# Optimization experiments

Hardware: AMD Instinct MI355X
Metric: run time of the kernel (lower is better)

Reference implementation:

```python
import jax, jax.numpy as jnp
import numpy as np

FEATURE_DIM = 512
NUM_NODES = 50
NUM_GCN_LAYERS = 2
H_IMG = W_IMG = 256


def setup_inputs() -> dict:
    key = jax.random.key(0)
    ks = jax.random.split(key, 14)
    s = lambda k, shape: (jax.random.normal(k, shape, jnp.float32) * 0.02)
    return {
        "fts": jax.random.normal(ks[0], (1, FEATURE_DIM, H_IMG, W_IMG), jnp.float32),
        "msk": jax.random.randint(ks[1], (1, H_IMG, W_IMG), 0, 2, jnp.int32),
        "gcn_w": s(ks[2], (NUM_GCN_LAYERS, FEATURE_DIM, FEATURE_DIM)),
        "gcn_b": s(ks[3], (NUM_GCN_LAYERS, FEATURE_DIM)),
        "q_w": s(ks[4], (FEATURE_DIM // 2, FEATURE_DIM)),
        "q_b": s(ks[5], (FEATURE_DIM // 2,)),
        "k_w": s(ks[6], (FEATURE_DIM // 2, FEATURE_DIM)),
        "k_b": s(ks[7], (FEATURE_DIM // 2,)),
        "v_w": s(ks[8], (FEATURE_DIM, FEATURE_DIM)),
        "v_b": s(ks[9], (FEATURE_DIM,)),
        "map_w": s(ks[10], (FEATURE_DIM, FEATURE_DIM)),
        "map_b": s(ks[11], (FEATURE_DIM,)),
        "gamma": jnp.float32(0.1),   # torch inits to 0; nonzero for coverage
        "alpha": jnp.float32(-4.0),  # matches torch init
    }


def _adaptive_avg_pool1d(x, n):
    """torch.nn.AdaptiveAvgPool1d over last axis. x: [C, L] -> [C, n].
    Bin i averages x[:, floor(i*L/n) : ceil((i+1)*L/n)]. Done via cumsum."""
    L = x.shape[-1]
    i = np.arange(n)
    starts = (i * L) // n
    ends = ((i + 1) * L + n - 1) // n  # ceil
    cs = jnp.concatenate([jnp.zeros(x.shape[:-1] + (1,), x.dtype), jnp.cumsum(x, axis=-1)], axis=-1)
    sums = cs[..., ends] - cs[..., starts]
    return sums / jnp.asarray(ends - starts, x.dtype)


def reference(fts, msk, gcn_w, gcn_b, q_w, q_b, k_w, k_b, v_w, v_b, map_w, map_b, gamma, alpha):
    # interpolate(fts, size=msk.shape[-2:]) is identity: sizes already match.
    msk_f = msk.astype(fts.dtype)                     # [1, H, W]
    m = msk_f[:, None]                                # [1, 1, H, W]
    glob_proto = jnp.sum(fts * m, axis=(-2, -1)) / (jnp.sum(msk_f) + 1e-8)  # [1, 512]

    # masked_select -> [512, L] foreground pixels (eager nonzero; msk is data)
    fg_idx = jnp.nonzero(msk.reshape(-1))[0]
    fg = fts.reshape(FEATURE_DIM, -1)[:, fg_idx]      # [512, L]
    local_protos = _adaptive_avg_pool1d(fg, NUM_NODES).T  # [50, 512]

    H = jnp.concatenate([glob_proto, local_protos], axis=0)  # [51, 512]
    for l in range(NUM_GCN_LAYERS):
        Hn = H / jnp.maximum(jnp.linalg.norm(H, axis=1, keepdims=True), 1e-12)
        adj = jax.nn.softmax(jnp.maximum(Hn @ Hn.T, 0.0), axis=1)  # [51, 51]
        agg = adj @ H
        H = H + jax.nn.relu(agg @ gcn_w[l].T + gcn_b[l])

    # cross-attention: q from node 0, k/v from remaining 50 nodes
    q_node, k_nodes = H[:1], H[1:]
    q = q_node @ q_w.T + q_b                          # [1, 256]
    k = k_nodes @ k_w.T + k_b                         # [50, 256]
    v = k_nodes @ v_w.T + v_b                         # [50, 512]
    attn = jax.nn.softmax((q @ k.T) / (q_w.shape[0] ** 0.5), axis=-1)
    final_proto = q_node + gamma * ((attn @ v) @ map_w.T + map_b)  # [1, 512]

    w = jax.nn.sigmoid(alpha)
    return glob_proto * (1 - w) + final_proto * w
```

## Files before the change

### kernel.cpp

```cpp
#include <hip/hip_runtime.h>

#define HW 65536
#define CDIM 512
#define NN 50
#define NROWS 51

__device__ __forceinline__ float wave_sum(float v) {
#pragma unroll
  for (int off = 32; off; off >>= 1) v += __shfl_xor(v, off, 64);
  return v;
}
__device__ __forceinline__ int wave_sum_i(int v) {
#pragma unroll
  for (int off = 32; off; off >>= 1) v += __shfl_xor(v, off, 64);
  return v;
}
__device__ __forceinline__ float wave_max(float v) {
#pragma unroll
  for (int off = 32; off; off >>= 1) v = fmaxf(v, __shfl_xor(v, off, 64));
  return v;
}

__global__ __launch_bounds__(256) void k_transpose(
    const float* g0, const float* g1, const float* qw, const float* kw,
    const float* vw, const float* mw,
    float* g0T, float* g1T, float* qwT, float* kwT, float* vwT, float* mwT) {
  const float* in; float* out; int rows, cols;
  switch (blockIdx.z) {
    case 0: in = g0; out = g0T; rows = 512; cols = 512; break;
    case 1: in = g1; out = g1T; rows = 512; cols = 512; break;
    case 2: in = qw; out = qwT; rows = 256; cols = 512; break;
    case 3: in = kw; out = kwT; rows = 256; cols = 512; break;
    case 4: in = vw; out = vwT; rows = 512; cols = 512; break;
    default: in = mw; out = mwT; rows = 512; cols = 512; break;
  }
  int c0 = blockIdx.x * 32, r0 = blockIdx.y * 32;
  if (r0 >= rows || c0 >= cols) return;
  __shared__ float tile[32][33];
  int tx = threadIdx.x, ty = threadIdx.y;
#pragma unroll
  for (int j = 0; j < 4; ++j)
    tile[ty + j * 8][tx] = in[(size_t)(r0 + ty + j * 8) * cols + c0 + tx];
  __syncthreads();
#pragma unroll
  for (int j = 0; j < 4; ++j)
    out[(size_t)(c0 + ty + j * 8) * rows + r0 + tx] = tile[tx][ty + j * 8];
}

__global__ __launch_bounds__(256) void k_count(const int* msk, int* blkcnt, float* seg) {
  int t = threadIdx.x, b = blockIdx.x;
  int g = b * 256 + t;
  if (g < NN * CDIM) seg[g] = 0.f;
  int g2 = g + 16384;
  if (g2 < NN * CDIM) seg[g2] = 0.f;
  int4 m = ((const int4*)msk)[g];
  int c = (m.x != 0) + (m.y != 0) + (m.z != 0) + (m.w != 0);
  c = wave_sum_i(c);
  __shared__ int wl[4];
  if ((t & 63) == 0) wl[t >> 6] = c;
  __syncthreads();
  if (t == 0) blkcnt[b] = wl[0] + wl[1] + wl[2] + wl[3];
}

__global__ void k_scan(const int* blkcnt, int* blkoff, int* meta) {
  int t = threadIdx.x;
  int c = blkcnt[t];
  int x = c;
#pragma unroll
  for (int d = 1; d < 64; d <<= 1) {
    int y = __shfl_up(x, d, 64);
    if (t >= d) x += y;
  }
  blkoff[t] = x - c;
  int L = __shfl(x, 63, 64);
  if (t == 0) meta[0] = L;
  if (t < NN) {
    long long Ll = L;
    int s = (int)((long long)t * Ll / NN);
    int e = (int)(((long long)(t + 1) * Ll + NN - 1) / NN);
    int sn = (int)((long long)(t + 1) * Ll / NN);
    meta[2 + t] = s;
    meta[2 + NN + t] = e - s;
    meta[2 + 2 * NN + t] = (t < NN - 1) ? (e > sn) : 0;
  }
}

__global__ __launch_bounds__(256) void k_rank(const int* msk, const int* blkoff,
                                              const int* meta, unsigned char* bin8, int* P) {
  int t = threadIdx.x, blk = blockIdx.x;
  int L = meta[0];
  __shared__ int sst[NN];
  __shared__ int wtot[4];
  if (t < NN) sst[t] = meta[2 + t];
  int4 m = ((const int4*)msk)[blk * 256 + t];
  int fl[4] = {m.x != 0, m.y != 0, m.z != 0, m.w != 0};
  int cnt = fl[0] + fl[1] + fl[2] + fl[3];
  int lane = t & 63, wv = t >> 6;
  int x = cnt;
#pragma unroll
  for (int d = 1; d < 64; d <<= 1) {
    int y = __shfl_up(x, d, 64);
    if (lane >= d) x += y;
  }
  if (lane == 63) wtot[wv] = x;
  __syncthreads();
  int base = blkoff[blk] + (x - cnt);
  for (int w = 0; w < wv; ++w) base += wtot[w];
  int p0 = blk * 1024 + t * 4;
  int r = base;
#pragma unroll
  for (int j = 0; j < 4; ++j) {
    int p = p0 + j;
    unsigned char bv = 255;
    if (fl[j]) {
      bv = (unsigned char)((long long)NN * r / L);
#pragma unroll 1
      for (int i = 0; i < NN; ++i)
        if (sst[i] == r) P[i] = p;
      r++;
    }
    bin8[p] = bv;
  }
}

__global__ __launch_bounds__(256) void k_seg(const float* __restrict__ fts,
                                             const unsigned char* __restrict__ bin8,
                                             float* __restrict__ seg) {
  int pb = blockIdx.x * 1024;
  int cwb = blockIdx.y * 64;
  int t = threadIdx.x, lane = t & 63, wv = t >> 6;
  __shared__ int sbm[2];
  if (t == 0) { sbm[0] = 255; sbm[1] = -1; }
  __syncthreads();
  uchar4 b4 = ((const uchar4*)bin8)[(pb >> 2) + t];
  int bb[4] = {b4.x, b4.y, b4.z, b4.w};
  int mn = 255, mx = -1;
#pragma unroll
  for (int j = 0; j < 4; ++j)
    if (bb[j] != 255) { mn = min(mn, bb[j]); mx = max(mx, bb[j]); }
  if (mn < 255) atomicMin(&sbm[0], mn);
  if (mx >= 0) atomicMax(&sbm[1], mx);
  __syncthreads();
  int bmin = sbm[0], bmax = sbm[1];
  if (bmax < 0) return;
  int cw = cwb + wv * 16;
  const float* base = fts + (size_t)cw * HW + pb + lane;
  const unsigned char* bp = bin8 + pb + lane;
  if (bmax - bmin <= 3) {
    float racc[16][4];
#pragma unroll
    for (int a = 0; a < 16; ++a)
#pragma unroll
      for (int j = 0; j < 4; ++j) racc[a][j] = 0.f;
#pragma unroll 1
    for (int it = 0; it < 16; ++it) {
      int b = bp[it * 64];
      int brel = b - bmin;
      bool k0 = brel == 0, k1 = brel == 1, k2 = brel == 2, k3 = brel == 3;
#pragma unroll
      for (int cs = 0; cs < 16; ++cs) {
        float v = base[(size_t)cs * HW + it * 64];
        racc[cs][0] += k0 ? v : 0.f;
        racc[cs][1] += k1 ? v : 0.f;
        racc[cs][2] += k2 ? v : 0.f;
        racc[cs][3] += k3 ? v : 0.f;
      }
    }
#pragma unroll 1
    for (int cs = 0; cs < 16; ++cs) {
#pragma unroll 1
      for (int j = 0; j < 4; ++j) {
        float v = wave_sum(racc[cs][j]);
        if (lane == 0 && v != 0.f) {
          int b = bmin + j;
          if (b < NN) atomicAdd(&seg[b * CDIM + cw + cs], v);
        }
      }
    }
  } else {
    for (int it = 0; it < 16; ++it) {
      int b = bp[it * 64];
      if (b == 255) continue;
      for (int cs = 0; cs < 16; ++cs) {
        float v = base[(size_t)cs * HW + it * 64];
        atomicAdd(&seg[b * CDIM + cw + cs], v);
      }
    }
  }
}

__global__ __launch_bounds__(512) void k_buildH(const float* fts, const float* seg,
                                                const int* meta, const int* P,
                                                float* glob, float* H, float* norms) {
  int r = blockIdx.x;
  int c = threadIdx.x;
  int L = meta[0];
  float h;
  if (r == 0) {
    float s = 0.f;
#pragma unroll 1
    for (int i = 0; i < NN; ++i) s += seg[i * CDIM + c];
    h = s / ((float)L + 1e-8f);
    glob[c] = h;
  } else {
    int i = r - 1;
    const int* cntv = meta + 2 + NN;
    const int* ov = meta + 2 + 2 * NN;
    float s = seg[i * CDIM + c];
    if (ov[i]) s += fts[(size_t)c * HW + P[i + 1]];
    h = s / fmaxf((float)cntv[i], 1.f);
  }
  H[r * CDIM + c] = h;
  float x = wave_sum(h * h);
  __shared__ float wsum[8];
  if ((c & 63) == 0) wsum[c >> 6] = x;
  __syncthreads();
  if (c == 0) {
    float s = 0.f;
    for (int w = 0; w < 8; ++w) s += wsum[w];
    norms[r] = fmaxf(sqrtf(s), 1e-12f);
  }
}

__global__ __launch_bounds__(256) void k_gcnA(const float* H, const float* norms, float* agg) {
  int a = blockIdx.x;
  int t = threadIdx.x, lane = t & 63, wv = t >> 6;
  __shared__ float sHa[CDIM];
  __shared__ float sadj[64];
  sHa[t] = H[a * CDIM + t];
  sHa[t + 256] = H[a * CDIM + t + 256];
  __syncthreads();
  float na = norms[a];
  for (int b = wv; b < NROWS; b += 4) {
    float d = 0.f;
#pragma unroll 2
    for (int k = lane; k < CDIM; k += 64) d += sHa[k] * H[b * CDIM + k];
    d = wave_sum(d);
    if (lane == 0) sadj[b] = fmaxf(d / (na * norms[b]), 0.f);
  }
  __syncthreads();
  if (t < 64) {
    float s = (t < NROWS) ? sadj[t] : -1e30f;
    float m = wave_max(s);
    float e = (t < NROWS) ? expf(s - m) : 0.f;
    float sum = wave_sum(e);
    if (t < NROWS) sadj[t] = e / sum;
  }
  __syncthreads();
  for (int c = t; c < CDIM; c += 256) {
    float acc = 0.f;
#pragma unroll 1
    for (int b = 0; b < NROWS; ++b) acc += sadj[b] * H[b * CDIM + c];
    agg[a * CDIM + c] = acc;
  }
}

__global__ __launch_bounds__(512) void k_gcnB(float* H, const float* agg,
                                              const float* WT, const float* bias,
                                              float* norms) {
  int r = blockIdx.x, c = threadIdx.x;
  __shared__ float sagg[CDIM];
  sagg[c] = agg[r * CDIM + c];
  __syncthreads();
  float acc = bias[c];
#pragma unroll 4
  for (int k = 0; k < CDIM; ++k) acc += sagg[k] * WT[k * CDIM + c];
  float h = H[r * CDIM + c] + fmaxf(acc, 0.f);
  H[r * CDIM + c] = h;
  float x = wave_sum(h * h);
  __shared__ float wsum[8];
  if ((c & 63) == 0) wsum[c >> 6] = x;
  __syncthreads();
  if (c == 0) {
    float s = 0.f;
    for (int w = 0; w < 8; ++w) s += wsum[w];
    norms[r] = fmaxf(sqrtf(s), 1e-12f);
  }
}

__global__ __launch_bounds__(256) void k_qkv(const float* H, const float* qwT,
                                             const float* kwT, const float* vwT,
                                             const float* qb, const float* kb, const float* vb,
                                             float* q, float* kk, float* vv) {
  int blk = blockIdx.x;
  int t = threadIdx.x;
  __shared__ float sh[CDIM];
  sh[t] = H[blk * CDIM + t];
  sh[t + 256] = H[blk * CDIM + t + 256];
  __syncthreads();
  if (blk == 0) {
    float acc = qb[t];
#pragma unroll 4
    for (int k = 0; k < CDIM; ++k) acc += sh[k] * qwT[k * 256 + t];
    q[t] = acc;
  } else {
    int i = blk - 1;
    float acc = kb[t];
#pragma unroll 4
    for (int k = 0; k < CDIM; ++k) acc += sh[k] * kwT[k * 256 + t];
    kk[i * 256 + t] = acc;
    float a0 = vb[t], a1 = vb[t + 256];
#pragma unroll 4
    for (int k = 0; k < CDIM; ++k) {
      float hv = sh[k];
      a0 += hv * vwT[k * CDIM + t];
      a1 += hv * vwT[k * CDIM + t + 256];
    }
    vv[i * CDIM + t] = a0;
    vv[i * CDIM + t + 256] = a1;
  }
}

__global__ __launch_bounds__(512) void k_final(const float* H, const float* glob,
                                               const float* q, const float* kk, const float* vv,
                                               const float* mapwT, const float* mapb,
                                               const float* gamma, const float* alpha,
                                               float* out) {
  int t = threadIdx.x, lane = t & 63, wv = t >> 6;
  __shared__ float sattn[64];
  __shared__ float sav[CDIM];
  for (int i = wv; i < NN; i += 8) {
    float d = 0.f;
#pragma unroll
    for (int k = lane; k < 256; k += 64) d += q[k] * kk[i * 256 + k];
    d = wave_sum(d);
    if (lane == 0) sattn[i] = d * (1.f / 16.f);
  }
  __syncthreads();
  if (t < 64) {
    float s = (t < NN) ? sattn[t] : -1e30f;
    float m = wave_max(s);
    float e = (t < NN) ? expf(s - m) : 0.f;
    float sum = wave_sum(e);
    if (t < NN) sattn[t] = e / sum;
  }
  __syncthreads();
  float av = 0.f;
#pragma unroll 1
  for (int i = 0; i < NN; ++i) av += sattn[i] * vv[i * CDIM + t];
  sav[t] = av;
  __syncthreads();
  float o = mapb[t];
#pragma unroll 4
  for (int k = 0; k < CDIM; ++k) o += sav[k] * mapwT[k * CDIM + t];
  float w = 1.f / (1.f + expf(-alpha[0]));
  float fp = H[t] + gamma[0] * o;
  out[t] = glob[t] * (1.f - w) + fp * w;
}

extern "C" void kernel_launch(void* const* d_in, const int* in_sizes, int n_in,
                              void* d_out, int out_size, void* d_ws, size_t ws_size,
                              hipStream_t stream) {
  const float* fts = (const float*)d_in[0];
  const int* msk = (const int*)d_in[1];
  const float* gcn_w = (const float*)d_in[2];
  const float* gcn_b = (const float*)d_in[3];
  const float* q_w = (const float*)d_in[4];
  const float* q_b = (const float*)d_in[5];
  const float* k_w = (const float*)d_in[6];
  const float* k_b = (const float*)d_in[7];
  const float* v_w = (const float*)d_in[8];
  const float* v_b = (const float*)d_in[9];
  const float* map_w = (const float*)d_in[10];
  const float* map_b = (const float*)d_in[11];
  const float* gamma = (const float*)d_in[12];
  const float* alpha = (const float*)d_in[13];
  float* out = (float*)d_out;

  char* w = (char*)d_ws;
  auto alloc = [&](size_t bytes) {
    char* p = w;
    w += (bytes + 255) & ~(size_t)255;
    return p;
  };
  float* g0T = (float*)alloc(512 * 512 * 4);
  float* g1T = (float*)alloc(512 * 512 * 4);
  float* qwT = (float*)alloc(512 * 256 * 4);
  float* kwT = (float*)alloc(512 * 256 * 4);
  float* vwT = (float*)alloc(512 * 512 * 4);
  float* mwT = (float*)alloc(512 * 512 * 4);
  int* blkcnt = (int*)alloc(64 * 4);
  int* blkoff = (int*)alloc(64 * 4);
  int* meta = (int*)alloc(160 * 4);
  int* P = (int*)alloc(NN * 4);
  unsigned char* bin8 = (unsigned char*)alloc(HW);
  float* seg = (float*)alloc(NN * CDIM * 4);
  float* glob = (float*)alloc(CDIM * 4);
  float* H = (float*)alloc(NROWS * CDIM * 4);
  float* norms = (float*)alloc(NROWS * 4);
  float* agg = (float*)alloc(NROWS * CDIM * 4);
  float* qv = (float*)alloc(256 * 4);
  float* kv = (float*)alloc(NN * 256 * 4);
  float* vv = (float*)alloc(NN * CDIM * 4);

  k_transpose<<<dim3(16, 16, 6), dim3(32, 8), 0, stream>>>(
      gcn_w, gcn_w + 512 * 512, q_w, k_w, v_w, map_w, g0T, g1T, qwT, kwT, vwT, mwT);
  k_count<<<64, 256, 0, stream>>>(msk, blkcnt, seg);
  k_scan<<<1, 64, 0, stream>>>(blkcnt, blkoff, meta);
  k_rank<<<64, 256, 0, stream>>>(msk, blkoff, meta, bin8, P);
  k_seg<<<dim3(64, 8), 256, 0, stream>>>(fts, bin8, seg);
  k_buildH<<<NROWS, 512, 0, stream>>>(fts, seg, meta, P, glob, H, norms);
  for (int l = 0; l < 2; ++l) {
    k_gcnA<<<NROWS, 256, 0, stream>>>(H, norms, agg);
    k_gcnB<<<NROWS, 512, 0, stream>>>(H, agg, l ? g1T : g0T, gcn_b + l * 512, norms);
  }
  k_qkv<<<NROWS, 256, 0, stream>>>(H, qwT, kwT, vwT, q_b, k_b, v_b, qv, kv, vv);
  k_final<<<1, 512, 0, stream>>>(H, glob, qv, kv, vv, mwT, map_b, gamma, alpha, out);
}
```

Measured before the change: 558.6 us.

## Fuse prep kernels, merge GCN stages, widen grids for seg and small GEMVs

Folds the mask count, seg zeroing and all weight transposes into one prep kernel, and moves the block scan inside k_rank. Pivot lookup becomes an O(1) index instead of a 50-entry loop. k_seg now uses 256-pixel blocks with float4 loads and wave-level min/max instead of shared atomics, giving four times more blocks. The two GCN kernels per layer merge into one and are split across four column slices, with ping-pong H buffers and atomic norm accumulation. qkv and final are also split over more blocks so the small GEMVs spread across more CUs. This cuts launch count and raises parallelism, but each GCN slice block recomputes the full adjacency and aggregation.

```diff
diff --git a/kernel.cpp b/kernel.cpp
--- a/kernel.cpp
+++ b/kernel.cpp
@@ -20,78 +20,94 @@
   for (int off = 32; off; off >>= 1) v = fmaxf(v, __shfl_xor(v, off, 64));
   return v;
 }
-
-__global__ __launch_bounds__(256) void k_transpose(
-    const float* g0, const float* g1, const float* qw, const float* kw,
-    const float* vw, const float* mw,
-    float* g0T, float* g1T, float* qwT, float* kwT, float* vwT, float* mwT) {
-  const float* in; float* out; int rows, cols;
-  switch (blockIdx.z) {
-    case 0: in = g0; out = g0T; rows = 512; cols = 512; break;
-    case 1: in = g1; out = g1T; rows = 512; cols = 512; break;
-    case 2: in = qw; out = qwT; rows = 256; cols = 512; break;
-    case 3: in = kw; out = kwT; rows = 256; cols = 512; break;
-    case 4: in = vw; out = vwT; rows = 512; cols = 512; break;
-    default: in = mw; out = mwT; rows = 512; cols = 512; break;
-  }
-  int c0 = blockIdx.x * 32, r0 = blockIdx.y * 32;
-  if (r0 >= rows || c0 >= cols) return;
+__device__ __forceinline__ int wave_max_i(int v) {
+#pragma unroll
+  for (int off = 32; off; off >>= 1) v = max(v, __shfl_xor(v, off, 64));
+  return v;
+}
+__device__ __forceinline__ int wave_min_i(int v) {
+#pragma unroll
+  for (int off = 32; off; off >>= 1) v = min(v, __shfl_xor(v, off, 64));
+  return v;
+}
+
+__global__ __launch_bounds__(256) void k_prep(
+    const int* __restrict__ msk, int* __restrict__ blkcnt, float* __restrict__ seg,
+    float* __restrict__ nsqB, float* __restrict__ nsqC,
+    const float* __restrict__ g0, const float* __restrict__ g1,
+    const float* __restrict__ qw, const float* __restrict__ kw,
+    const float* __restrict__ vw, const float* __restrict__ mw,
+    float* __restrict__ g0T, float* __restrict__ g1T, float* __restrict__ qwT,
+    float* __restrict__ kwT, float* __restrict__ vwT, float* __restrict__ mwT) {
+  int t = threadIdx.x, b = blockIdx.x;
   __shared__ float tile[32][33];
-  int tx = threadIdx.x, ty = threadIdx.y;
-#pragma unroll
-  for (int j = 0; j < 4; ++j)
-    tile[ty + j * 8][tx] = in[(size_t)(r0 + ty + j * 8) * cols + c0 + tx];
-  __syncthreads();
-#pragma unroll
-  for (int j = 0; j < 4; ++j)
-    out[(size_t)(c0 + ty + j * 8) * rows + r0 + tx] = tile[tx][ty + j * 8];
-}
-
-__global__ __launch_bounds__(256) void k_count(const int* msk, int* blkcnt, float* seg) {
-  int t = threadIdx.x, b = blockIdx.x;
-  int g = b * 256 + t;
-  if (g < NN * CDIM) seg[g] = 0.f;
-  int g2 = g + 16384;
-  if (g2 < NN * CDIM) seg[g2] = 0.f;
-  int4 m = ((const int4*)msk)[g];
-  int c = (m.x != 0) + (m.y != 0) + (m.z != 0) + (m.w != 0);
-  c = wave_sum_i(c);
   __shared__ int wl[4];
-  if ((t & 63) == 0) wl[t >> 6] = c;
-  __syncthreads();
-  if (t == 0) blkcnt[b] = wl[0] + wl[1] + wl[2] + wl[3];
-}
-
-__global__ void k_scan(const int* blkcnt, int* blkoff, int* meta) {
-  int t = threadIdx.x;
-  int c = blkcnt[t];
-  int x = c;
-#pragma unroll
-  for (int d = 1; d < 64; d <<= 1) {
-    int y = __shfl_up(x, d, 64);
-    if (t >= d) x += y;
-  }
-  blkoff[t] = x - c;
-  int L = __shfl(x, 63, 64);
-  if (t == 0) meta[0] = L;
-  if (t < NN) {
+  if (b < 64) {
+    int g = b * 256 + t;
+    if (g < NN * CDIM) seg[g] = 0.f;
+    int g2 = g + 16384;
+    if (g2 < NN * CDIM) seg[g2] = 0.f;
+    if (b == 0 && t < NROWS) { nsqB[t] = 0.f; nsqC[t] = 0.f; }
+    int4 m = ((const int4*)msk)[g];
+    int c = (m.x != 0) + (m.y != 0) + (m.z != 0) + (m.w != 0);
+    c = wave_sum_i(c);
+    if ((t & 63) == 0) wl[t >> 6] = c;
+    __syncthreads();
+    if (t == 0) blkcnt[b] = wl[0] + wl[1] + wl[2] + wl[3];
+  } else {
+    int tid = b - 64;
+    const float* in; float* out; int rows, cols, lt;
+    if (tid < 256)       { in = g0; out = g0T; rows = 512; cols = 512; lt = tid; }
+    else if (tid < 512)  { in = g1; out = g1T; rows = 512; cols = 512; lt = tid - 256; }
+    else if (tid < 640)  { in = qw; out = qwT; rows = 256; cols = 512; lt = tid - 512; }
+    else if (tid < 768)  { in = kw; out = kwT; rows = 256; cols = 512; lt = tid - 640; }
+    else if (tid < 1024) { in = vw; out = vwT; rows = 512; cols = 512; lt = tid - 768; }
+    else                 { in = mw; out = mwT; rows = 512; cols = 512; lt = tid - 1024; }
+    int ctiles = cols / 32;
+    int r0 = (lt / ctiles) * 32, c0 = (lt % ctiles) * 32;
+    int tx = t & 31, ty = t >> 5;
+#pragma unroll
+    for (int j = 0; j < 4; ++j)
+      tile[ty + j * 8][tx] = in[(size_t)(r0 + ty + j * 8) * cols + c0 + tx];
+    __syncthreads();
+#pragma unroll
+    for (int j = 0; j < 4; ++j)
+      out[(size_t)(c0 + ty + j * 8) * rows + r0 + tx] = tile[tx][ty + j * 8];
+  }
+}
+
+__global__ __launch_bounds__(256) void k_rank(const int* __restrict__ msk,
+                                              const int* __restrict__ blkcnt,
+                                              int* __restrict__ meta,
+                                              unsigned char* __restrict__ bin8,
+                                              int* __restrict__ P) {
+  int t = threadIdx.x, blk = blockIdx.x;
+  __shared__ int sblkoff, sL;
+  __shared__ int sst[NN + 1];
+  __shared__ int wtot[4];
+  if (t < 64) {
+    int c = blkcnt[t];
+    int x = c;
+#pragma unroll
+    for (int d = 1; d < 64; d <<= 1) {
+      int y = __shfl_up(x, d, 64);
+      if (t >= d) x += y;
+    }
+    if (t == blk) sblkoff = x - c;
+    if (t == 63) sL = x;
+  }
+  __syncthreads();
+  int L = sL;
+  if (t <= NN) sst[t] = (int)((long long)t * L / NN);
+  if (blk == 0 && t < NN) {
+    if (t == 0) meta[0] = L;
     long long Ll = L;
     int s = (int)((long long)t * Ll / NN);
     int e = (int)(((long long)(t + 1) * Ll + NN - 1) / NN);
-    int sn = (int)((long long)(t + 1) * Ll / NN);
-    meta[2 + t] = s;
+    int ci = (int)(((long long)t * Ll + NN - 1) / NN);
     meta[2 + NN + t] = e - s;
-    meta[2 + 2 * NN + t] = (t < NN - 1) ? (e > sn) : 0;
-  }
-}
-
-__global__ __launch_bounds__(256) void k_rank(const int* msk, const int* blkoff,
-                                              const int* meta, unsigned char* bin8, int* P) {
-  int t = threadIdx.x, blk = blockIdx.x;
-  int L = meta[0];
-  __shared__ int sst[NN];
-  __shared__ int wtot[4];
-  if (t < NN) sst[t] = meta[2 + t];
+    meta[2 + 2 * NN + t] = (t >= 1 && ci > s) ? 1 : 0;
+  }
   int4 m = ((const int4*)msk)[blk * 256 + t];
   int fl[4] = {m.x != 0, m.y != 0, m.z != 0, m.w != 0};
   int cnt = fl[0] + fl[1] + fl[2] + fl[3];
@@ -104,7 +120,7 @@
   }
   if (lane == 63) wtot[wv] = x;
   __syncthreads();
-  int base = blkoff[blk] + (x - cnt);
+  int base = sblkoff + (x - cnt);
   for (int w = 0; w < wv; ++w) base += wtot[w];
   int p0 = blk * 1024 + t * 4;
   int r = base;
@@ -113,10 +129,10 @@
     int p = p0 + j;
     unsigned char bv = 255;
     if (fl[j]) {
-      bv = (unsigned char)((long long)NN * r / L);
-#pragma unroll 1
-      for (int i = 0; i < NN; ++i)
-        if (sst[i] == r) P[i] = p;
+      int bi = (int)((long long)NN * r / L);
+      bv = (unsigned char)bi;
+      if (sst[bi] == r) P[bi] = p;
+      if (bi + 1 < NN && sst[bi + 1] == r) P[bi + 1] = p;
       r++;
     }
     bin8[p] = bv;
@@ -126,89 +142,82 @@
 __global__ __launch_bounds__(256) void k_seg(const float* __restrict__ fts,
                                              const unsigned char* __restrict__ bin8,
                                              float* __restrict__ seg) {
-  int pb = blockIdx.x * 1024;
-  int cwb = blockIdx.y * 64;
+  int pb = blockIdx.x * 256;
   int t = threadIdx.x, lane = t & 63, wv = t >> 6;
-  __shared__ int sbm[2];
-  if (t == 0) { sbm[0] = 255; sbm[1] = -1; }
-  __syncthreads();
-  uchar4 b4 = ((const uchar4*)bin8)[(pb >> 2) + t];
+  int cw = blockIdx.y * 64 + wv * 16;
+  uchar4 b4 = *(const uchar4*)(bin8 + pb + lane * 4);
   int bb[4] = {b4.x, b4.y, b4.z, b4.w};
   int mn = 255, mx = -1;
 #pragma unroll
   for (int j = 0; j < 4; ++j)
     if (bb[j] != 255) { mn = min(mn, bb[j]); mx = max(mx, bb[j]); }
-  if (mn < 255) atomicMin(&sbm[0], mn);
-  if (mx >= 0) atomicMax(&sbm[1], mx);
-  __syncthreads();
-  int bmin = sbm[0], bmax = sbm[1];
-  if (bmax < 0) return;
-  int cw = cwb + wv * 16;
-  const float* base = fts + (size_t)cw * HW + pb + lane;
-  const unsigned char* bp = bin8 + pb + lane;
-  if (bmax - bmin <= 3) {
+  mn = wave_min_i(mn);
+  mx = wave_max_i(mx);
+  if (mx < 0) return;
+  const float* base = fts + (size_t)cw * HW + pb + lane * 4;
+  int span = mx - mn;
+  if (span <= 3) {
+    int br0 = bb[0] - mn, br1 = bb[1] - mn, br2 = bb[2] - mn, br3 = bb[3] - mn;
     float racc[16][4];
 #pragma unroll
     for (int a = 0; a < 16; ++a)
 #pragma unroll
       for (int j = 0; j < 4; ++j) racc[a][j] = 0.f;
-#pragma unroll 1
-    for (int it = 0; it < 16; ++it) {
-      int b = bp[it * 64];
-      int brel = b - bmin;
-      bool k0 = brel == 0, k1 = brel == 1, k2 = brel == 2, k3 = brel == 3;
-#pragma unroll
-      for (int cs = 0; cs < 16; ++cs) {
-        float v = base[(size_t)cs * HW + it * 64];
-        racc[cs][0] += k0 ? v : 0.f;
-        racc[cs][1] += k1 ? v : 0.f;
-        racc[cs][2] += k2 ? v : 0.f;
-        racc[cs][3] += k3 ? v : 0.f;
-      }
+#pragma unroll 8
+    for (int cs = 0; cs < 16; ++cs) {
+      float4 v = *(const float4*)(base + (size_t)cs * HW);
+      racc[cs][0] += (br0 == 0 ? v.x : 0.f) + (br1 == 0 ? v.y : 0.f) +
+                     (br2 == 0 ? v.z : 0.f) + (br3 == 0 ? v.w : 0.f);
+      racc[cs][1] += (br0 == 1 ? v.x : 0.f) + (br1 == 1 ? v.y : 0.f) +
+                     (br2 == 1 ? v.z : 0.f) + (br3 == 1 ? v.w : 0.f);
+      racc[cs][2] += (br0 == 2 ? v.x : 0.f) + (br1 == 2 ? v.y : 0.f) +
+                     (br2 == 2 ? v.z : 0.f) + (br3 == 2 ? v.w : 0.f);
+      racc[cs][3] += (br0 == 3 ? v.x : 0.f) + (br1 == 3 ? v.y : 0.f) +
+                     (br2 == 3 ? v.z : 0.f) + (br3 == 3 ? v.w : 0.f);
     }
 #pragma unroll 1
     for (int cs = 0; cs < 16; ++cs) {
-#pragma unroll 1
+#pragma unroll
       for (int j = 0; j < 4; ++j) {
-        float v = wave_sum(racc[cs][j]);
-        if (lane == 0 && v != 0.f) {
-          int b = bmin + j;
-          if (b < NN) atomicAdd(&seg[b * CDIM + cw + cs], v);
+        if (j <= span) {
+          float s = wave_sum(racc[cs][j]);
+          if (lane == 0 && s != 0.f) atomicAdd(&seg[(mn + j) * CDIM + cw + cs], s);
         }
       }
     }
   } else {
-    for (int it = 0; it < 16; ++it) {
-      int b = bp[it * 64];
-      if (b == 255) continue;
-      for (int cs = 0; cs < 16; ++cs) {
-        float v = base[(size_t)cs * HW + it * 64];
-        atomicAdd(&seg[b * CDIM + cw + cs], v);
-      }
-    }
-  }
-}
-
-__global__ __launch_bounds__(512) void k_buildH(const float* fts, const float* seg,
-                                                const int* meta, const int* P,
-                                                float* glob, float* H, float* norms) {
-  int r = blockIdx.x;
-  int c = threadIdx.x;
+#pragma unroll 1
+    for (int cs = 0; cs < 16; ++cs) {
+      float4 v = *(const float4*)(base + (size_t)cs * HW);
+      float vs[4] = {v.x, v.y, v.z, v.w};
+#pragma unroll
+      for (int j = 0; j < 4; ++j)
+        if (bb[j] != 255) atomicAdd(&seg[bb[j] * CDIM + cw + cs], vs[j]);
+    }
+  }
+}
+
+__global__ __launch_bounds__(512) void k_buildH(const float* __restrict__ fts,
+                                                const float* __restrict__ seg,
+                                                const int* __restrict__ meta,
+                                                const int* __restrict__ P,
+                                                float* __restrict__ glob,
+                                                float* __restrict__ H,
+                                                float* __restrict__ nsq) {
+  int r = blockIdx.x, c = threadIdx.x;
   int L = meta[0];
   float h;
   if (r == 0) {
     float s = 0.f;
-#pragma unroll 1
+#pragma unroll 5
     for (int i = 0; i < NN; ++i) s += seg[i * CDIM + c];
     h = s / ((float)L + 1e-8f);
     glob[c] = h;
   } else {
     int i = r - 1;
-    const int* cntv = meta + 2 + NN;
-    const int* ov = meta + 2 + 2 * NN;
     float s = seg[i * CDIM + c];
-    if (ov[i]) s += fts[(size_t)c * HW + P[i + 1]];
-    h = s / fmaxf((float)cntv[i], 1.f);
+    if (meta[2 + 2 * NN + i]) s += fts[(size_t)c * HW + P[i]];
+    h = s / fmaxf((float)meta[2 + NN + i], 1.f);
   }
   H[r * CDIM + c] = h;
   float x = wave_sum(h * h);
@@ -217,135 +226,151 @@
   __syncthreads();
   if (c == 0) {
     float s = 0.f;
+#pragma unroll
     for (int w = 0; w < 8; ++w) s += wsum[w];
-    norms[r] = fmaxf(sqrtf(s), 1e-12f);
-  }
-}
-
-__global__ __launch_bounds__(256) void k_gcnA(const float* H, const float* norms, float* agg) {
-  int a = blockIdx.x;
-  int t = threadIdx.x, lane = t & 63, wv = t >> 6;
+    nsq[r] = s;
+  }
+}
+
+__global__ __launch_bounds__(128) void k_gcn(const float* __restrict__ Hin,
+                                             const float* __restrict__ nsqIn,
+                                             float* __restrict__ Hout,
+                                             float* __restrict__ nsqOut,
+                                             const float* __restrict__ WT,
+                                             const float* __restrict__ bias) {
+  int a = blockIdx.x, s = blockIdx.y;
+  int t = threadIdx.x, lane = t & 63, w = t >> 6;
   __shared__ float sHa[CDIM];
   __shared__ float sadj[64];
-  sHa[t] = H[a * CDIM + t];
-  sHa[t + 256] = H[a * CDIM + t + 256];
-  __syncthreads();
-  float na = norms[a];
-  for (int b = wv; b < NROWS; b += 4) {
+  __shared__ float sagg[CDIM];
+#pragma unroll
+  for (int i = 0; i < 4; ++i) sHa[t + i * 128] = Hin[a * CDIM + t + i * 128];
+  __syncthreads();
+  float na = fmaxf(sqrtf(nsqIn[a]), 1e-12f);
+  for (int b = w; b < NROWS; b += 2) {
     float d = 0.f;
-#pragma unroll 2
-    for (int k = lane; k < CDIM; k += 64) d += sHa[k] * H[b * CDIM + k];
+    const float* hb = Hin + b * CDIM;
+#pragma unroll
+    for (int k = 0; k < 8; ++k) d += sHa[lane + k * 64] * hb[lane + k * 64];
     d = wave_sum(d);
-    if (lane == 0) sadj[b] = fmaxf(d / (na * norms[b]), 0.f);
+    if (lane == 0) {
+      float nb = fmaxf(sqrtf(nsqIn[b]), 1e-12f);
+      sadj[b] = fmaxf(d / (na * nb), 0.f);
+    }
   }
   __syncthreads();
   if (t < 64) {
-    float s = (t < NROWS) ? sadj[t] : -1e30f;
-    float m = wave_max(s);
-    float e = (t < NROWS) ? expf(s - m) : 0.f;
+    float sv = (t < NROWS) ? sadj[t] : -1e30f;
+    float m = wave_max(sv);
+    float e = (t < NROWS) ? expf(sv - m) : 0.f;
     float sum = wave_sum(e);
     if (t < NROWS) sadj[t] = e / sum;
   }
   __syncthreads();
-  for (int c = t; c < CDIM; c += 256) {
+#pragma unroll
+  for (int ci = 0; ci < 4; ++ci) {
+    int c = t + ci * 128;
     float acc = 0.f;
-#pragma unroll 1
-    for (int b = 0; b < NROWS; ++b) acc += sadj[b] * H[b * CDIM + c];
-    agg[a * CDIM + c] = acc;
-  }
-}
-
-__global__ __launch_bounds__(512) void k_gcnB(float* H, const float* agg,
-                                              const float* WT, const float* bias,
-                                              float* norms) {
-  int r = blockIdx.x, c = threadIdx.x;
-  __shared__ float sagg[CDIM];
-  sagg[c] = agg[r * CDIM + c];
-  __syncthreads();
+#pragma unroll 3
+    for (int b = 0; b < NROWS; ++b) acc += sadj[b] * Hin[b * CDIM + c];
+    sagg[c] = acc;
+  }
+  __syncthreads();
+  int c = s * 128 + t;
   float acc = bias[c];
-#pragma unroll 4
+#pragma unroll 16
   for (int k = 0; k < CDIM; ++k) acc += sagg[k] * WT[k * CDIM + c];
-  float h = H[r * CDIM + c] + fmaxf(acc, 0.f);
-  H[r * CDIM + c] = h;
-  float x = wave_sum(h * h);
-  __shared__ float wsum[8];
-  if ((c & 63) == 0) wsum[c >> 6] = x;
-  __syncthreads();
-  if (c == 0) {
-    float s = 0.f;
-    for (int w = 0; w < 8; ++w) s += wsum[w];
-    norms[r] = fmaxf(sqrtf(s), 1e-12f);
-  }
-}
-
-__global__ __launch_bounds__(256) void k_qkv(const float* H, const float* qwT,
-                                             const float* kwT, const float* vwT,
-                                             const float* qb, const float* kb, const float* vb,
-                                             float* q, float* kk, float* vv) {
-  int blk = blockIdx.x;
-  int t = threadIdx.x;
+  float h = sHa[c] + fmaxf(acc, 0.f);
+  Hout[a * CDIM + c] = h;
+  float p = wave_sum(h * h);
+  if (lane == 0) atomicAdd(&nsqOut[a], p);
+}
+
+__global__ __launch_bounds__(128) void k_qkv(const float* __restrict__ H,
+                                             const float* __restrict__ qwT,
+                                             const float* __restrict__ kwT,
+                                             const float* __restrict__ vwT,
+                                             const float* __restrict__ qb,
+                                             const float* __restrict__ kb,
+                                             const float* __restrict__ vb,
+                                             float* __restrict__ q,
+                                             float* __restrict__ kk,
+                                             float* __restrict__ vv) {
+  int a = blockIdx.x, s = blockIdx.y, t = threadIdx.x;
   __shared__ float sh[CDIM];
-  sh[t] = H[blk * CDIM + t];
-  sh[t + 256] = H[blk * CDIM + t + 256];
-  __syncthreads();
-  if (blk == 0) {
-    float acc = qb[t];
-#pragma unroll 4
-    for (int k = 0; k < CDIM; ++k) acc += sh[k] * qwT[k * 256 + t];
-    q[t] = acc;
+#pragma unroll
+  for (int i = 0; i < 4; ++i) sh[t + i * 128] = H[a * CDIM + t + i * 128];
+  __syncthreads();
+  if (a == 0) {
+    if (t < 64) {
+      int c = s * 64 + t;
+      float acc = qb[c];
+#pragma unroll 16
+      for (int k = 0; k < CDIM; ++k) acc += sh[k] * qwT[k * 256 + c];
+      q[c] = acc;
+    }
   } else {
-    int i = blk - 1;
-    float acc = kb[t];
-#pragma unroll 4
-    for (int k = 0; k < CDIM; ++k) acc += sh[k] * kwT[k * 256 + t];
-    kk[i * 256 + t] = acc;
-    float a0 = vb[t], a1 = vb[t + 256];
-#pragma unroll 4
-    for (int k = 0; k < CDIM; ++k) {
-      float hv = sh[k];
-      a0 += hv * vwT[k * CDIM + t];
-      a1 += hv * vwT[k * CDIM + t + 256];
-    }
-    vv[i * CDIM + t] = a0;
-    vv[i * CDIM + t + 256] = a1;
-  }
-}
-
-__global__ __launch_bounds__(512) void k_final(const float* H, const float* glob,
-                                               const float* q, const float* kk, const float* vv,
-                                               const float* mapwT, const float* mapb,
-                                               const float* gamma, const float* alpha,
-                                               float* out) {
-  int t = threadIdx.x, lane = t & 63, wv = t >> 6;
+    int i = a - 1;
+    if (t < 64) {
+      int c = s * 64 + t;
+      float acc = kb[c];
+#pragma unroll 16
+      for (int k = 0; k < CDIM; ++k) acc += sh[k] * kwT[k * 256 + c];
+      kk[i * 256 + c] = acc;
+    }
+    int c = s * 128 + t;
+    float acc = vb[c];
+#pragma unroll 16
+    for (int k = 0; k < CDIM; ++k) acc += sh[k] * vwT[k * CDIM + c];
+    vv[i * CDIM + c] = acc;
+  }
+}
+
+__global__ __launch_bounds__(128) void k_final(const float* __restrict__ H,
+                                               const float* __restrict__ glob,
+                                               const float* __restrict__ q,
+                                               const float* __restrict__ kk,
+                                               const float* __restrict__ vv,
+                                               const float* __restrict__ mwT,
+                                               const float* __restrict__ mapb,
+                                               const float* __restrict__ gamma,
+                                               const float* __restrict__ alpha,
+                                               float* __restrict__ out) {
+  int t = threadIdx.x, lane = t & 63, w = t >> 6;
   __shared__ float sattn[64];
   __shared__ float sav[CDIM];
-  for (int i = wv; i < NN; i += 8) {
+  for (int i = w; i < NN; i += 2) {
     float d = 0.f;
 #pragma unroll
-    for (int k = lane; k < 256; k += 64) d += q[k] * kk[i * 256 + k];
+    for (int k = 0; k < 4; ++k) d += q[lane + k * 64] * kk[i * 256 + lane + k * 64];
     d = wave_sum(d);
     if (lane == 0) sattn[i] = d * (1.f / 16.f);
   }
   __syncthreads();
   if (t < 64) {
-    float s = (t < NN) ? sattn[t] : -1e30f;
-    float m = wave_max(s);
-    float e = (t < NN) ? expf(s - m) : 0.f;
+    float sv = (t < NN) ? sattn[t] : -1e30f;
+    float m = wave_max(sv);
+    float e = (t < NN) ? expf(sv - m) : 0.f;
     float sum = wave_sum(e);
     if (t < NN) sattn[t] = e / sum;
   }
   __syncthreads();
-  float av = 0.f;
-#pragma unroll 1
-  for (int i = 0; i < NN; ++i) av += sattn[i] * vv[i * CDIM + t];
-  sav[t] = av;
-  __syncthreads();
-  float o = mapb[t];
-#pragma unroll 4
-  for (int k = 0; k < CDIM; ++k) o += sav[k] * mapwT[k * CDIM + t];
-  float w = 1.f / (1.f + expf(-alpha[0]));
-  float fp = H[t] + gamma[0] * o;
-  out[t] = glob[t] * (1.f - w) + fp * w;
+#pragma unroll
+  for (int ci = 0; ci < 4; ++ci) {
+    int c = t + ci * 128;
+    float acc = 0.f;
+#pragma unroll 5
+    for (int i = 0; i < NN; ++i) acc += sattn[i] * vv[i * CDIM + c];
+    sav[c] = acc;
+  }
+  __syncthreads();
+  int c = blockIdx.x * 128 + t;
+  float o = mapb[c];
+#pragma unroll 16
+  for (int k = 0; k < CDIM; ++k) o += sav[k] * mwT[k * CDIM + c];
+  float wv_ = 1.f / (1.f + expf(-alpha[0]));
+  float fp = H[c] + gamma[0] * o;
+  out[c] = glob[c] * (1.f - wv_) + fp * wv_;
 }
 
 extern "C" void kernel_launch(void* const* d_in, const int* in_sizes, int n_in,
@@ -367,10 +392,10 @@
   const float* alpha = (const float*)d_in[13];
   float* out = (float*)d_out;
 
-  char* w = (char*)d_ws;
+  char* wp = (char*)d_ws;
   auto alloc = [&](size_t bytes) {
-    char* p = w;
-    w += (bytes + 255) & ~(size_t)255;
+    char* p = wp;
+    wp += (bytes + 255) & ~(size_t)255;
     return p;
   };
   float* g0T = (float*)alloc(512 * 512 * 4);
@@ -380,30 +405,29 @@
   float* vwT = (float*)alloc(512 * 512 * 4);
   float* mwT = (float*)alloc(512 * 512 * 4);
   int* blkcnt = (int*)alloc(64 * 4);
-  int* blkoff = (int*)alloc(64 * 4);
   int* meta = (int*)alloc(160 * 4);
   int* P = (int*)alloc(NN * 4);
   unsigned char* bin8 = (unsigned char*)alloc(HW);
   float* seg = (float*)alloc(NN * CDIM * 4);
   float* glob = (float*)alloc(CDIM * 4);
-  float* H = (float*)alloc(NROWS * CDIM * 4);
-  float* norms = (float*)alloc(NROWS * 4);
-  float* agg = (float*)alloc(NROWS * CDIM * 4);
+  float* HA = (float*)alloc(NROWS * CDIM * 4);
+  float* HB = (float*)alloc(NROWS * CDIM * 4);
+  float* HC = (float*)alloc(NROWS * CDIM * 4);
+  float* nsqA = (float*)alloc(NROWS * 4);
+  float* nsqB = (float*)alloc(NROWS * 4);
+  float* nsqC = (float*)alloc(NROWS * 4);
   float* qv = (float*)alloc(256 * 4);
   float* kv = (float*)alloc(NN * 256 * 4);
   float* vv = (float*)alloc(NN * CDIM * 4);
 
-  k_transpose<<<dim3(16, 16, 6), dim3(32, 8), 0, stream>>>(
-      gcn_w, gcn_w + 512 * 512, q_w, k_w, v_w, map_w, g0T, g1T, qwT, kwT, vwT, mwT);
-  k_count<<<64, 256, 0, stream>>>(msk, blkcnt, seg);
-  k_scan<<<1, 64, 0, stream>>>(blkcnt, blkoff, meta);
-  k_rank<<<64, 256, 0, stream>>>(msk, blkoff, meta, bin8, P);
-  k_seg<<<dim3(64, 8), 256, 0, stream>>>(fts, bin8, seg);
-  k_buildH<<<NROWS, 512, 0, stream>>>(fts, seg, meta, P, glob, H, norms);
-  for (int l = 0; l < 2; ++l) {
-    k_gcnA<<<NROWS, 256, 0, stream>>>(H, norms, agg);
-    k_gcnB<<<NROWS, 512, 0, stream>>>(H, agg, l ? g1T : g0T, gcn_b + l * 512, norms);
-  }
-  k_qkv<<<NROWS, 256, 0, stream>>>(H, qwT, kwT, vwT, q_b, k_b, v_b, qv, kv, vv);
-  k_final<<<1, 512, 0, stream>>>(H, glob, qv, kv, vv, mwT, map_b, gamma, alpha, out);
-}
+  k_prep<<<1344, 256, 0, stream>>>(msk, blkcnt, seg, nsqB, nsqC,
+                                   gcn_w, gcn_w + 512 * 512, q_w, k_w, v_w, map_w,
+                                   g0T, g1T, qwT, kwT, vwT, mwT);
+  k_rank<<<64, 256, 0, stream>>>(msk, blkcnt, meta, bin8, P);
+  k_seg<<<dim3(256, 8), 256, 0, stream>>>(fts, bin8, seg);
+  k_buildH<<<NROWS, 512, 0, stream>>>(fts, seg, meta, P, glob, HA, nsqA);
+  k_gcn<<<dim3(NROWS, 4), 128, 0, stream>>>(HA, nsqA, HB, nsqB, g0T, gcn_b);
+  k_gcn<<<dim3(NROWS, 4), 128, 0, stream>>>(HB, nsqB, HC, nsqC, g1T, gcn_b + 512);
+  k_qkv<<<dim3(NROWS, 4), 128, 0, stream>>>(HC, qwT, kwT, vwT, q_b, k_b, v_b, qv, kv, vv);
+  k_final<<<4, 128, 0, stream>>>(HC, glob, qv, kv, vv, mwT, map_b, gamma, alpha, out);
+}
```

Result: faster. 454.2 us (-18.7%).
